# Performance work log

Hardware: AMD Instinct MI355X
Metric: run time of the kernel (lower is better)

## Reference

```python
import jax, jax.numpy as jnp
import numpy as np
import math

HIDDEN = 1024
N_HEADS = 16
HEAD = HIDDEN // N_HEADS

def setup_inputs() -> dict:
    key = jax.random.key(0)
    k1, k2, k3 = jax.random.split(key, 3)
    encodings = jax.random.normal(k1, (2, 2048, HIDDEN), dtype=jnp.float32)
    W_attn = jax.random.normal(k2, (HIDDEN, 3 * HIDDEN), dtype=jnp.float32) * 0.02
    b_attn = jnp.zeros((3 * HIDDEN,), dtype=jnp.float32)
    W_out = jax.random.normal(k3, (HIDDEN, HIDDEN), dtype=jnp.float32) * 0.02
    b_out = jnp.zeros((HIDDEN,), dtype=jnp.float32)
    return {"encodings": encodings, "W_attn": W_attn, "b_attn": b_attn,
            "W_out": W_out, "b_out": b_out}

def reference(encodings, W_attn, b_attn, W_out, b_out):
    b, n, _ = encodings.shape
    qkv = encodings @ W_attn + b_attn              # [b, n, 3*hidden]
    q, k, v = jnp.split(qkv, 3, axis=-1)
    # 'b n (h l) -> b h n l'
    def to_heads(t):
        return t.reshape(b, n, N_HEADS, HEAD).transpose(0, 2, 1, 3)
    q, k, v = to_heads(q), to_heads(k), to_heads(v)
    # scores[b,h,k,q]; causal mask keeps key_pos <= query_pos
    scores = jnp.einsum('bhki,bhqi->bhkq', k, q) / math.sqrt(HEAD)
    mask = jnp.arange(n)[:, None] <= jnp.arange(n)[None, :]   # [k, q]
    scores = jnp.where(mask, scores, jnp.float32(-10000.0))
    attn = jax.nn.softmax(scores, axis=2)          # softmax over key dim
    combined = jnp.einsum('bhkq,bhkl->bhql', attn, v)  # [b, h, n, head]
    out = combined.transpose(0, 2, 1, 3).reshape(b, n, HIDDEN)
    return out @ W_out + b_out
```

## Files before the change

### kernel.cpp

```cpp
#include <hip/hip_runtime.h>
#include <hip/hip_bf16.h>

typedef __attribute__((ext_vector_type(8))) short bf16x8;
typedef __attribute__((ext_vector_type(4))) short bf16x4;
typedef __attribute__((ext_vector_type(4))) float f32x4;

__device__ __forceinline__ short f2bf(float f) {
    unsigned u = __float_as_uint(f);
    u += 0x7fff + ((u >> 16) & 1);
    return (short)(u >> 16);
}
__device__ __forceinline__ float bf2f(short s) {
    return __uint_as_float(((unsigned)(unsigned short)s) << 16);
}
__device__ __forceinline__ unsigned pk_bf16(float lo, float hi) {
    __hip_bfloat162 t = __float22bfloat162_rn(make_float2(lo, hi));
    unsigned u;
    __builtin_memcpy(&u, &t, 4);
    return u;
}

#define GLOAD_LDS16(gp, lp)                                                            \
    __builtin_amdgcn_global_load_lds(                                                  \
        (const __attribute__((address_space(1))) unsigned*)(gp),                       \
        (__attribute__((address_space(3))) unsigned*)(lp), 16, 0, 0)

#define QK_SCALE 0.180336879f
#define MFMA16(a, b, c) __builtin_amdgcn_mfma_f32_16x16x32_bf16((a), (b), (c), 0, 0, 0)

__device__ __forceinline__ void tcvt_tile(const float* __restrict__ W, short* __restrict__ Wt,
                                          int K, int N, int bx, int by, int t,
                                          short (*tile)[72]) {
    const int k0 = by * 64, n0 = bx * 64;
    #pragma unroll
    for (int jj = 0; jj < 4; ++jj) {
        int row = jj * 16 + (t >> 4);
        int col = (t & 15) * 4;
        f32x4 v = *(const f32x4*)&W[(size_t)(k0 + row) * N + n0 + col];
        bf16x4 b = {f2bf(v.x), f2bf(v.y), f2bf(v.z), f2bf(v.w)};
        *(bf16x4*)&tile[row][col] = b;
    }
    __syncthreads();
    const int nr = t >> 2, kc = (t & 3) * 16;
    bf16x8 o0, o1;
    #pragma unroll
    for (int j = 0; j < 8; ++j) { o0[j] = tile[kc + j][nr]; o1[j] = tile[kc + 8 + j][nr]; }
    short* dst = &Wt[(size_t)(n0 + nr) * K + k0 + kc];
    *(bf16x8*)dst = o0;
    *(bf16x8*)(dst + 8) = o1;
}

__global__ __launch_bounds__(256) void prep_kernel(
    const float* __restrict__ enc, const float* __restrict__ Wa,
    const float* __restrict__ ba, const float* __restrict__ Wo,
    const float* __restrict__ bo, short* __restrict__ Abf,
    short* __restrict__ WtA, short* __restrict__ bbA,
    short* __restrict__ WtO, short* __restrict__ bbO)
{
    __shared__ alignas(16) short tile[64][72];
    const int id = blockIdx.x, t = threadIdx.x;
    if (id < 2048) {
        const int i = id * 2048 + t * 8;
        f32x4 a = *(const f32x4*)&enc[i];
        f32x4 b = *(const f32x4*)&enc[i + 4];
        bf16x8 o = {f2bf(a.x), f2bf(a.y), f2bf(a.z), f2bf(a.w),
                    f2bf(b.x), f2bf(b.y), f2bf(b.z), f2bf(b.w)};
        *(bf16x8*)&Abf[i] = o;
    } else if (id == 2048) {
        for (int j = t * 8; j < 3072; j += 2048) {
            f32x4 a = *(const f32x4*)&ba[j];
            f32x4 b = *(const f32x4*)&ba[j + 4];
            bf16x8 o = {f2bf(a.x), f2bf(a.y), f2bf(a.z), f2bf(a.w),
                        f2bf(b.x), f2bf(b.y), f2bf(b.z), f2bf(b.w)};
            *(bf16x8*)&bbA[j] = o;
        }
    } else if (id == 2049) {
        if (t < 128) {
            const int j = t * 8;
            f32x4 a = *(const f32x4*)&bo[j];
            f32x4 b = *(const f32x4*)&bo[j + 4];
            bf16x8 o = {f2bf(a.x), f2bf(a.y), f2bf(a.z), f2bf(a.w),
                        f2bf(b.x), f2bf(b.y), f2bf(b.z), f2bf(b.w)};
            *(bf16x8*)&bbO[j] = o;
        }
        __syncthreads();
    } else if (id < 2818) {
        const int lid = id - 2050;
        tcvt_tile(Wa, WtA, 1024, 3072, lid % 48, lid / 48, t, tile);
    } else {
        const int lid = id - 2818;
        tcvt_tile(Wo, WtO, 1024, 1024, lid % 16, lid / 16, t, tile);
    }
}

template<int BN, bool F32OUT, bool SPLIT3>
__global__ __launch_bounds__(256) void gemm_bt(
    const short* __restrict__ A, const short* __restrict__ Bt,
    const short* __restrict__ bias, void* __restrict__ C,
    short* __restrict__ Kw, short* __restrict__ Vw, int M, int N, int K)
{
    __shared__ alignas(16) short LB[128 * 64 + BN * 64];
    short* As = LB;
    short* Bs = LB + 128 * 64;
    short* Ct = LB;

    const int tid = threadIdx.x, w = tid >> 6, lane = tid & 63;
    const int quad = lane >> 4, l16 = lane & 15;
    constexpr int MT = (BN == 128) ? 4 : 2;
    const int wm = (BN == 128) ? (w >> 1) : w;
    const int wn = (BN == 128) ? (w & 1) : 0;
    const int m0 = blockIdx.y * 128, n0 = blockIdx.x * BN;
    const int srow = lane >> 3;
    const int scol = ((lane & 7) ^ srow) * 8;

    f32x4 acc[MT][4] = {};

    for (int k0 = 0; k0 < K; k0 += 64) {
        __syncthreads();
        #pragma unroll
        for (int jj = 0; jj < 4; ++jj) {
            const int rb = w * 32 + jj * 8;
            GLOAD_LDS16(&A[(size_t)(m0 + rb + srow) * K + k0 + scol], &As[rb * 64]);
        }
        if (BN == 128) {
            #pragma unroll
            for (int jj = 0; jj < 4; ++jj) {
                const int rb = w * 32 + jj * 8;
                GLOAD_LDS16(&Bt[(size_t)(n0 + rb + srow) * K + k0 + scol], &Bs[rb * 64]);
            }
        } else {
            #pragma unroll
            for (int jj = 0; jj < 2; ++jj) {
                const int rb = w * 16 + jj * 8;
                GLOAD_LDS16(&Bt[(size_t)(n0 + rb + srow) * K + k0 + scol], &Bs[rb * 64]);
            }
        }
        __syncthreads();
        #pragma unroll
        for (int half = 0; half < 2; ++half) {
            const int kc2 = half * 4 + quad;
            bf16x8 af[MT], bfr[4];
            #pragma unroll
            for (int i = 0; i < MT; ++i) {
                const int row = wm * (MT * 16) + i * 16 + l16;
                af[i] = *(const bf16x8*)&As[row * 64 + ((kc2 ^ (row & 7)) << 3)];
            }
            #pragma unroll
            for (int i = 0; i < 4; ++i) {
                const int row = wn * 64 + i * 16 + l16;
                bfr[i] = *(const bf16x8*)&Bs[row * 64 + ((kc2 ^ (row & 7)) << 3)];
            }
            #pragma unroll
            for (int mt = 0; mt < MT; ++mt)
                #pragma unroll
                for (int nt = 0; nt < 4; ++nt)
                    acc[mt][nt] = MFMA16(af[mt], bfr[nt], acc[mt][nt]);
        }
    }

    if (SPLIT3) {
        const int g = n0 >> 10;
        const int lc0 = n0 & 1023;
        __syncthreads();
        if (g < 2) {
            #pragma unroll
            for (int nt = 0; nt < 4; ++nt) {
                const int col = wn * 64 + nt * 16 + l16;
                const float bv = bf2f(bias[n0 + col]);
                const int chunk = col >> 3, wi = col & 7;
                #pragma unroll
                for (int mt = 0; mt < 4; ++mt) {
                    const int rbase = wm * 64 + mt * 16 + quad * 4;
                    #pragma unroll
                    for (int r = 0; r < 4; ++r) {
                        const int row = rbase + r;
                        float v = acc[mt][nt][r] + bv;
                        if (g == 0) v *= QK_SCALE;
                        Ct[row * 128 + (((chunk ^ (row & 15)) << 3) | wi)] = f2bf(v);
                    }
                }
            }
        } else {
            #pragma unroll
            for (int nt = 0; nt < 4; ++nt) {
                const int d = wn * 64 + nt * 16 + l16;
                const float bv = bf2f(bias[n0 + d]);
                const int dsw = d & 15;
                #pragma unroll
                for (int mt = 0; mt < 4; ++mt) {
                    const int key0 = wm * 64 + mt * 16 + quad * 4;
                    bf16x4 p = {f2bf(acc[mt][nt][0] + bv), f2bf(acc[mt][nt][1] + bv),
                                f2bf(acc[mt][nt][2] + bv), f2bf(acc[mt][nt][3] + bv)};
                    *(bf16x4*)&Ct[d * 128 + ((((key0 >> 3) ^ dsw) << 3) | (key0 & 7))] = p;
                }
            }
        }
        __syncthreads();
        const int batch = m0 >> 11;
        const int kc0 = (m0 & 2047) >> 6;
        const int head0 = lc0 >> 6;
        if (g == 0) {
            short* dst = (short*)C;
            #pragma unroll
            for (int i = 0; i < 8; ++i) {
                const int idx = i * 256 + tid;
                const int row = idx >> 4, chunk = idx & 15;
                bf16x8 v = *(const bf16x8*)&Ct[row * 128 + ((chunk ^ (row & 15)) << 3)];
                *(bf16x8*)&dst[(size_t)(m0 + row) * 1024 + lc0 + chunk * 8] = v;
            }
        } else if (g == 1) {
            #pragma unroll
            for (int i = 0; i < 8; ++i) {
                const int idx = i * 256 + tid;
                const int qd = idx >> 9, c = idx & 511;
                const int kcL = qd >> 1, headL = qd & 1;
                const int s = c >> 7, h2 = (c >> 6) & 1;
                const int l16c = c & 15, quadc = (c >> 4) & 3;
                const int row = kcL * 64 + s * 16 + l16c;
                const int colc = headL * 8 + h2 * 4 + quadc;
                bf16x8 v = *(const bf16x8*)&Ct[row * 128 + ((colc ^ (row & 15)) << 3)];
                const int bh = batch * 16 + head0 + headL, kc = kc0 + kcL;
                *(bf16x8*)&Kw[((size_t)(bh * 32 + kc) * 512 + c) * 8] = v;
            }
        } else {
            #pragma unroll
            for (int i = 0; i < 8; ++i) {
                const int idx = i * 256 + tid;
                const int qd = idx >> 9, c = idx & 511;
                const int kcL = qd >> 1, headL = qd & 1;
                const int h2 = c >> 8, dt = (c >> 6) & 3;
                const int l16c = c & 15, quadc = (c >> 4) & 3;
                const int d = headL * 64 + dt * 16 + l16c;
                const int keyc = kcL * 8 + h2 * 4 + quadc;
                bf16x8 v = *(const bf16x8*)&Ct[d * 128 + ((keyc ^ (d & 15)) << 3)];
                const int bh = batch * 16 + head0 + headL, kc = kc0 + kcL;
                *(bf16x8*)&Vw[((size_t)(bh * 32 + kc) * 512 + c) * 8] = v;
            }
        }
    } else {
        #pragma unroll
        for (int nt = 0; nt < 4; ++nt) {
            const int col = n0 + wn * 64 + nt * 16 + l16;
            const float bv = bf2f(bias[col]);
            #pragma unroll
            for (int mt = 0; mt < MT; ++mt) {
                const int row = m0 + wm * (MT * 16) + mt * 16 + quad * 4;
                #pragma unroll
                for (int r = 0; r < 4; ++r) {
                    float v = acc[mt][nt][r] + bv;
                    if (F32OUT) ((float*)C)[(size_t)(row + r) * N + col] = v;
                    else        ((short*)C)[(size_t)(row + r) * N + col] = f2bf(v);
                }
            }
        }
    }
}

__global__ __launch_bounds__(256) void attn_kernel(
    const short* __restrict__ Qw, const short* __restrict__ Kx,
    const short* __restrict__ Vx, short* __restrict__ comb)
{
    __shared__ alignas(16) short Ps[4][2][16 * 72];
    __shared__ alignas(16) float cbuf[2][2][64][16];
    __shared__ float clacc[2][2][64];

    const int tid = threadIdx.x, w4 = tid >> 6, lane = tid & 63;
    const int w = w4 & 1;
    const int h = w4 >> 1;
    const int quad = lane >> 4, l16 = lane & 15;
    const int bh = blockIdx.x;
    const int tA = blockIdx.y, tB = 63 - tA;
    const int batch = bh >> 4, head = bh & 15;
    const size_t rowbase = (size_t)batch * 2048;
    const int hcol = head * 64;
    const int q0A = tA * 32 + w * 16, q0B = tB * 32 + w * 16;
    const int diagA = tA >> 1, diagB = tB >> 1;
    const short* Kxbh = Kx + (size_t)bh * 131072;
    const short* Vxbh = Vx + (size_t)bh * 131072;
    const int lofs = lane * 8;
    short* pwA = &Ps[w4][0][0];
    short* pwB = &Ps[w4][1][0];

    bf16x8 qfA[2], qfB[2];
    {
        const short* pa = &Qw[(rowbase + q0A + l16) * 1024 + hcol];
        const short* pb = &Qw[(rowbase + q0B + l16) * 1024 + hcol];
        qfA[0] = *(const bf16x8*)(pa + quad * 8);
        qfA[1] = *(const bf16x8*)(pa + 32 + quad * 8);
        qfB[0] = *(const bf16x8*)(pb + quad * 8);
        qfB[1] = *(const bf16x8*)(pb + 32 + quad * 8);
    }

    f32x4 otA[4] = {}, otB[4] = {};
    float laccA = 0.f, laccB = 0.f;

    bf16x8 kf[4][2];
    {
        const short* kb0 = Kxbh + (size_t)h * 4096;
        #pragma unroll
        for (int s = 0; s < 4; ++s) {
            kf[s][0] = *(const bf16x8*)&kb0[(s * 2 + 0) * 512 + lofs];
            kf[s][1] = *(const bf16x8*)&kb0[(s * 2 + 1) * 512 + lofs];
        }
    }

    for (int kc = h; kc <= diagB; kc += 2) {
        const bool actA = (kc <= diagA);
        const int key0 = kc * 64;

        const short* vb = Vxbh + (size_t)kc * 4096;
        bf16x8 vf[2][4];
        #pragma unroll
        for (int hh = 0; hh < 2; ++hh)
            #pragma unroll
            for (int dt = 0; dt < 4; ++dt)
                vf[hh][dt] = *(const bf16x8*)&vb[(hh * 4 + dt) * 512 + lofs];

        f32x4 svA[4], svB[4];
        #pragma unroll
        for (int s = 0; s < 4; ++s) {
            f32x4 a = {0.f, 0.f, 0.f, 0.f};
            a = MFMA16(kf[s][0], qfB[0], a);
            a = MFMA16(kf[s][1], qfB[1], a);
            svB[s] = a;
            if (actA) {
                f32x4 b = {0.f, 0.f, 0.f, 0.f};
                b = MFMA16(kf[s][0], qfA[0], b);
                b = MFMA16(kf[s][1], qfA[1], b);
                svA[s] = b;
            }
        }

        if (kc + 2 <= diagB) {
            const short* kb = Kxbh + (size_t)(kc + 2) * 4096;
            #pragma unroll
            for (int s = 0; s < 4; ++s) {
                kf[s][0] = *(const bf16x8*)&kb[(s * 2 + 0) * 512 + lofs];
                kf[s][1] = *(const bf16x8*)&kb[(s * 2 + 1) * 512 + lofs];
            }
        }

        if (kc == diagB) {
            const int qq = q0B + l16;
            #pragma unroll
            for (int s = 0; s < 4; ++s) {
                const int keyb = key0 + s * 16 + quad * 4;
                #pragma unroll
                for (int r = 0; r < 4; ++r)
                    svB[s][r] = (keyb + r <= qq) ? svB[s][r] : -1e30f;
            }
        }
        #pragma unroll
        for (int s = 0; s < 4; ++s) {
            #pragma unroll
            for (int r = 0; r < 4; ++r) svB[s][r] = exp2f(svB[s][r]);
            laccB += (svB[s][0] + svB[s][1]) + (svB[s][2] + svB[s][3]);
            *(unsigned*)&pwB[l16 * 72 + s * 16 + quad * 4]     = pk_bf16(svB[s][0], svB[s][1]);
            *(unsigned*)&pwB[l16 * 72 + s * 16 + quad * 4 + 2] = pk_bf16(svB[s][2], svB[s][3]);
        }
        if (actA) {
            if (kc == diagA) {
                const int qq = q0A + l16;
                #pragma unroll
                for (int s = 0; s < 4; ++s) {
                    const int keyb = key0 + s * 16 + quad * 4;
                    #pragma unroll
                    for (int r = 0; r < 4; ++r)
                        svA[s][r] = (keyb + r <= qq) ? svA[s][r] : -1e30f;
                }
            }
            #pragma unroll
            for (int s = 0; s < 4; ++s) {
                #pragma unroll
                for (int r = 0; r < 4; ++r) svA[s][r] = exp2f(svA[s][r]);
                laccA += (svA[s][0] + svA[s][1]) + (svA[s][2] + svA[s][3]);
                *(unsigned*)&pwA[l16 * 72 + s * 16 + quad * 4]     = pk_bf16(svA[s][0], svA[s][1]);
                *(unsigned*)&pwA[l16 * 72 + s * 16 + quad * 4 + 2] = pk_bf16(svA[s][2], svA[s][3]);
            }
        }

        {
            bf16x8 pfB0 = *(const bf16x8*)&pwB[l16 * 72 + quad * 8];
            bf16x8 pfB1 = *(const bf16x8*)&pwB[l16 * 72 + 32 + quad * 8];
            #pragma unroll
            for (int dt = 0; dt < 4; ++dt) {
                otB[dt] = MFMA16(vf[0][dt], pfB0, otB[dt]);
                otB[dt] = MFMA16(vf[1][dt], pfB1, otB[dt]);
            }
            if (actA) {
                bf16x8 pfA0 = *(const bf16x8*)&pwA[l16 * 72 + quad * 8];
                bf16x8 pfA1 = *(const bf16x8*)&pwA[l16 * 72 + 32 + quad * 8];
                #pragma unroll
                for (int dt = 0; dt < 4; ++dt) {
                    otA[dt] = MFMA16(vf[0][dt], pfA0, otA[dt]);
                    otA[dt] = MFMA16(vf[1][dt], pfA1, otA[dt]);
                }
            }
        }
    }

    __syncthreads();
    if (h == 1) {
        #pragma unroll
        for (int dt = 0; dt < 4; ++dt) {
            *(f32x4*)&cbuf[w][0][lane][dt * 4] = otA[dt];
            *(f32x4*)&cbuf[w][1][lane][dt * 4] = otB[dt];
        }
        clacc[w][0][lane] = laccA;
        clacc[w][1][lane] = laccB;
    }
    __syncthreads();
    if (h == 0) {
        #pragma unroll
        for (int dt = 0; dt < 4; ++dt) {
            otA[dt] += *(const f32x4*)&cbuf[w][0][lane][dt * 4];
            otB[dt] += *(const f32x4*)&cbuf[w][1][lane][dt * 4];
        }
        laccA += clacc[w][0][lane];
        laccB += clacc[w][1][lane];

        laccA += __shfl_xor(laccA, 16);
        laccA += __shfl_xor(laccA, 32);
        laccB += __shfl_xor(laccB, 16);
        laccB += __shfl_xor(laccB, 32);
        const float invA = 1.0f / laccA, invB = 1.0f / laccB;

        #pragma unroll
        for (int dt = 0; dt < 4; ++dt) {
            *(unsigned*)&pwA[l16 * 72 + dt * 16 + quad * 4]     = pk_bf16(otA[dt][0] * invA, otA[dt][1] * invA);
            *(unsigned*)&pwA[l16 * 72 + dt * 16 + quad * 4 + 2] = pk_bf16(otA[dt][2] * invA, otA[dt][3] * invA);
            *(unsigned*)&pwB[l16 * 72 + dt * 16 + quad * 4]     = pk_bf16(otB[dt][0] * invB, otB[dt][1] * invB);
            *(unsigned*)&pwB[l16 * 72 + dt * 16 + quad * 4 + 2] = pk_bf16(otB[dt][2] * invB, otB[dt][3] * invB);
        }
        {
            const int qr = lane >> 2, dc = (lane & 3) * 16;
            bf16x8 a0 = *(const bf16x8*)&pwA[qr * 72 + dc];
            bf16x8 a1 = *(const bf16x8*)&pwA[qr * 72 + dc + 8];
            short* dstA = &comb[(rowbase + q0A + qr) * 1024 + hcol + dc];
            *(bf16x8*)dstA = a0;
            *(bf16x8*)(dstA + 8) = a1;
            bf16x8 b0 = *(const bf16x8*)&pwB[qr * 72 + dc];
            bf16x8 b1 = *(const bf16x8*)&pwB[qr * 72 + dc + 8];
            short* dstB = &comb[(rowbase + q0B + qr) * 1024 + hcol + dc];
            *(bf16x8*)dstB = b0;
            *(bf16x8*)(dstB + 8) = b1;
        }
    }
}

extern "C" void kernel_launch(void* const* d_in, const int* in_sizes, int n_in,
                              void* d_out, int out_size, void* d_ws, size_t ws_size,
                              hipStream_t stream)
{
    const float* enc = (const float*)d_in[0];
    const float* Wa  = (const float*)d_in[1];
    const float* ba  = (const float*)d_in[2];
    const float* Wo  = (const float*)d_in[3];
    const float* bo  = (const float*)d_in[4];
    float* out = (float*)d_out;

    char* ws = (char*)d_ws;
    short* Abf  = (short*)ws;
    short* comb = (short*)ws;
    short* WtO  = (short*)(ws + ((size_t)8 << 20));
    short* bbA  = (short*)(ws + ((size_t)10 << 20));
    short* bbO  = (short*)(ws + ((size_t)10 << 20) + 16384);
    short* WtA  = (short*)(ws + ((size_t)11 << 20));
    short* Kx   = (short*)(ws + ((size_t)17 << 20));
    short* Vx   = (short*)(ws + ((size_t)25 << 20));
    short* Qw   = (short*)(ws + ((size_t)33 << 20));

    prep_kernel<<<3074, 256, 0, stream>>>(enc, Wa, ba, Wo, bo, Abf, WtA, bbA, WtO, bbO);
    gemm_bt<128, false, true><<<dim3(24, 32), 256, 0, stream>>>(
        Abf, WtA, bbA, Qw, Kx, Vx, 4096, 3072, 1024);
    attn_kernel<<<dim3(32, 32), 256, 0, stream>>>(Qw, Kx, Vx, comb);
    gemm_bt<64, true, false><<<dim3(16, 32), 256, 0, stream>>>(
        comb, WtO, bbO, out, nullptr, nullptr, 4096, 1024, 1024);
}
```

Before: 187.5 us.

## Stage K/V tiles in shared LDS with double buffering across four attention waves

Each attention block now handles two query-tile pairs. All four waves walk the full key range instead of splitting key chunks by parity, so the cross-wave partial-sum reduction through shared memory goes away. K and V chunks are loaded once per block into double-buffered LDS with global_load_lds, and the next chunk is prefetched while the current one is computed. This replaces the per-wave global loads of the same K/V data. The attention grid is halved. The cost is a block-wide barrier every key-chunk iteration and fewer resident blocks to hide latency.

```diff
diff --git a/kernel.cpp b/kernel.cpp
--- a/kernel.cpp
+++ b/kernel.cpp
@@ -260,21 +260,22 @@
     const short* __restrict__ Qw, const short* __restrict__ Kx,
     const short* __restrict__ Vx, short* __restrict__ comb)
 {
+    __shared__ alignas(16) short KV[2][2][4096];
     __shared__ alignas(16) short Ps[4][2][16 * 72];
-    __shared__ alignas(16) float cbuf[2][2][64][16];
-    __shared__ float clacc[2][2][64];
 
     const int tid = threadIdx.x, w4 = tid >> 6, lane = tid & 63;
+    const int p = w4 >> 1;
     const int w = w4 & 1;
-    const int h = w4 >> 1;
     const int quad = lane >> 4, l16 = lane & 15;
     const int bh = blockIdx.x;
-    const int tA = blockIdx.y, tB = 63 - tA;
+    const int g = blockIdx.y;
+    const int tA = 2 * g + p, tB = 63 - tA;
     const int batch = bh >> 4, head = bh & 15;
     const size_t rowbase = (size_t)batch * 2048;
     const int hcol = head * 64;
     const int q0A = tA * 32 + w * 16, q0B = tB * 32 + w * 16;
-    const int diagA = tA >> 1, diagB = tB >> 1;
+    const int diagA = g;
+    const int maxD = 31 - g;
     const short* Kxbh = Kx + (size_t)bh * 131072;
     const short* Vxbh = Vx + (size_t)bh * 131072;
     const int lofs = lane * 8;
@@ -294,27 +295,37 @@
     f32x4 otA[4] = {}, otB[4] = {};
     float laccA = 0.f, laccB = 0.f;
 
-    bf16x8 kf[4][2];
+    const int sbase = w4 * 64;
+
     {
-        const short* kb0 = Kxbh + (size_t)h * 4096;
-        #pragma unroll
-        for (int s = 0; s < 4; ++s) {
-            kf[s][0] = *(const bf16x8*)&kb0[(s * 2 + 0) * 512 + lofs];
-            kf[s][1] = *(const bf16x8*)&kb0[(s * 2 + 1) * 512 + lofs];
-        }
-    }
-
-    for (int kc = h; kc <= diagB; kc += 2) {
+        #pragma unroll
+        for (int j = 0; j < 2; ++j) {
+            GLOAD_LDS16(&Kxbh[(size_t)(j * 256 + sbase + lane) * 8], &KV[0][0][(j * 256 + sbase) * 8]);
+            GLOAD_LDS16(&Vxbh[(size_t)(j * 256 + sbase + lane) * 8], &KV[0][1][(j * 256 + sbase) * 8]);
+        }
+    }
+    __syncthreads();
+
+    int cur = 0;
+    for (int kc = 0; kc <= maxD; ++kc) {
         const bool actA = (kc <= diagA);
         const int key0 = kc * 64;
 
-        const short* vb = Vxbh + (size_t)kc * 4096;
-        bf16x8 vf[2][4];
-        #pragma unroll
-        for (int hh = 0; hh < 2; ++hh)
-            #pragma unroll
-            for (int dt = 0; dt < 4; ++dt)
-                vf[hh][dt] = *(const bf16x8*)&vb[(hh * 4 + dt) * 512 + lofs];
+        if (kc < maxD) {
+            const size_t nb = (size_t)(kc + 1) * 4096;
+            #pragma unroll
+            for (int j = 0; j < 2; ++j) {
+                GLOAD_LDS16(&Kxbh[nb + (size_t)(j * 256 + sbase + lane) * 8], &KV[cur ^ 1][0][(j * 256 + sbase) * 8]);
+                GLOAD_LDS16(&Vxbh[nb + (size_t)(j * 256 + sbase + lane) * 8], &KV[cur ^ 1][1][(j * 256 + sbase) * 8]);
+            }
+        }
+
+        bf16x8 kf[4][2];
+        #pragma unroll
+        for (int s = 0; s < 4; ++s) {
+            kf[s][0] = *(const bf16x8*)&KV[cur][0][(s * 2 + 0) * 512 + lofs];
+            kf[s][1] = *(const bf16x8*)&KV[cur][0][(s * 2 + 1) * 512 + lofs];
+        }
 
         f32x4 svA[4], svB[4];
         #pragma unroll
@@ -331,16 +342,14 @@
             }
         }
 
-        if (kc + 2 <= diagB) {
-            const short* kb = Kxbh + (size_t)(kc + 2) * 4096;
-            #pragma unroll
-            for (int s = 0; s < 4; ++s) {
-                kf[s][0] = *(const bf16x8*)&kb[(s * 2 + 0) * 512 + lofs];
-                kf[s][1] = *(const bf16x8*)&kb[(s * 2 + 1) * 512 + lofs];
-            }
-        }
-
-        if (kc == diagB) {
+        bf16x8 vf[2][4];
+        #pragma unroll
+        for (int hh = 0; hh < 2; ++hh)
+            #pragma unroll
+            for (int dt = 0; dt < 4; ++dt)
+                vf[hh][dt] = *(const bf16x8*)&KV[cur][1][(hh * 4 + dt) * 512 + lofs];
+
+        if (kc == maxD) {
             const int qq = q0B + l16;
             #pragma unroll
             for (int s = 0; s < 4; ++s) {
@@ -397,54 +406,36 @@
                 }
             }
         }
-    }
-
-    __syncthreads();
-    if (h == 1) {
-        #pragma unroll
-        for (int dt = 0; dt < 4; ++dt) {
-            *(f32x4*)&cbuf[w][0][lane][dt * 4] = otA[dt];
-            *(f32x4*)&cbuf[w][1][lane][dt * 4] = otB[dt];
-        }
-        clacc[w][0][lane] = laccA;
-        clacc[w][1][lane] = laccB;
-    }
-    __syncthreads();
-    if (h == 0) {
-        #pragma unroll
-        for (int dt = 0; dt < 4; ++dt) {
-            otA[dt] += *(const f32x4*)&cbuf[w][0][lane][dt * 4];
-            otB[dt] += *(const f32x4*)&cbuf[w][1][lane][dt * 4];
-        }
-        laccA += clacc[w][0][lane];
-        laccB += clacc[w][1][lane];
-
-        laccA += __shfl_xor(laccA, 16);
-        laccA += __shfl_xor(laccA, 32);
-        laccB += __shfl_xor(laccB, 16);
-        laccB += __shfl_xor(laccB, 32);
-        const float invA = 1.0f / laccA, invB = 1.0f / laccB;
-
-        #pragma unroll
-        for (int dt = 0; dt < 4; ++dt) {
-            *(unsigned*)&pwA[l16 * 72 + dt * 16 + quad * 4]     = pk_bf16(otA[dt][0] * invA, otA[dt][1] * invA);
-            *(unsigned*)&pwA[l16 * 72 + dt * 16 + quad * 4 + 2] = pk_bf16(otA[dt][2] * invA, otA[dt][3] * invA);
-            *(unsigned*)&pwB[l16 * 72 + dt * 16 + quad * 4]     = pk_bf16(otB[dt][0] * invB, otB[dt][1] * invB);
-            *(unsigned*)&pwB[l16 * 72 + dt * 16 + quad * 4 + 2] = pk_bf16(otB[dt][2] * invB, otB[dt][3] * invB);
-        }
-        {
-            const int qr = lane >> 2, dc = (lane & 3) * 16;
-            bf16x8 a0 = *(const bf16x8*)&pwA[qr * 72 + dc];
-            bf16x8 a1 = *(const bf16x8*)&pwA[qr * 72 + dc + 8];
-            short* dstA = &comb[(rowbase + q0A + qr) * 1024 + hcol + dc];
-            *(bf16x8*)dstA = a0;
-            *(bf16x8*)(dstA + 8) = a1;
-            bf16x8 b0 = *(const bf16x8*)&pwB[qr * 72 + dc];
-            bf16x8 b1 = *(const bf16x8*)&pwB[qr * 72 + dc + 8];
-            short* dstB = &comb[(rowbase + q0B + qr) * 1024 + hcol + dc];
-            *(bf16x8*)dstB = b0;
-            *(bf16x8*)(dstB + 8) = b1;
-        }
+
+        __syncthreads();
+        cur ^= 1;
+    }
+
+    laccA += __shfl_xor(laccA, 16);
+    laccA += __shfl_xor(laccA, 32);
+    laccB += __shfl_xor(laccB, 16);
+    laccB += __shfl_xor(laccB, 32);
+    const float invA = 1.0f / laccA, invB = 1.0f / laccB;
+
+    #pragma unroll
+    for (int dt = 0; dt < 4; ++dt) {
+        *(unsigned*)&pwA[l16 * 72 + dt * 16 + quad * 4]     = pk_bf16(otA[dt][0] * invA, otA[dt][1] * invA);
+        *(unsigned*)&pwA[l16 * 72 + dt * 16 + quad * 4 + 2] = pk_bf16(otA[dt][2] * invA, otA[dt][3] * invA);
+        *(unsigned*)&pwB[l16 * 72 + dt * 16 + quad * 4]     = pk_bf16(otB[dt][0] * invB, otB[dt][1] * invB);
+        *(unsigned*)&pwB[l16 * 72 + dt * 16 + quad * 4 + 2] = pk_bf16(otB[dt][2] * invB, otB[dt][3] * invB);
+    }
+    {
+        const int qr = lane >> 2, dc = (lane & 3) * 16;
+        bf16x8 a0 = *(const bf16x8*)&pwA[qr * 72 + dc];
+        bf16x8 a1 = *(const bf16x8*)&pwA[qr * 72 + dc + 8];
+        short* dstA = &comb[(rowbase + q0A + qr) * 1024 + hcol + dc];
+        *(bf16x8*)dstA = a0;
+        *(bf16x8*)(dstA + 8) = a1;
+        bf16x8 b0 = *(const bf16x8*)&pwB[qr * 72 + dc];
+        bf16x8 b1 = *(const bf16x8*)&pwB[qr * 72 + dc + 8];
+        short* dstB = &comb[(rowbase + q0B + qr) * 1024 + hcol + dc];
+        *(bf16x8*)dstB = b0;
+        *(bf16x8*)(dstB + 8) = b1;
     }
 }
 
@@ -473,7 +464,7 @@
     prep_kernel<<<3074, 256, 0, stream>>>(enc, Wa, ba, Wo, bo, Abf, WtA, bbA, WtO, bbO);
     gemm_bt<128, false, true><<<dim3(24, 32), 256, 0, stream>>>(
         Abf, WtA, bbA, Qw, Kx, Vx, 4096, 3072, 1024);
-    attn_kernel<<<dim3(32, 32), 256, 0, stream>>>(Qw, Kx, Vx, comb);
+    attn_kernel<<<dim3(32, 16), 256, 0, stream>>>(Qw, Kx, Vx, comb);
     gemm_bt<64, true, false><<<dim3(16, 32), 256, 0, stream>>>(
         comb, WtO, bbO, out, nullptr, nullptr, 4096, 1024, 1024);
 }
```

Measured after the change: 190.0 us. About the same (+1.3%).
